# Performance work log

Hardware: AMD Instinct MI355X
Metric: run time of the kernel (lower is better)

## Reference

```python
import jax, jax.numpy as jnp
import numpy as np

N = 2048  # number of graph nodes


def setup_inputs() -> dict:
    key = jax.random.key(0)
    k1, k2, k3, k4 = jax.random.split(key, 4)
    # dense non-negative adjacency / association matrix
    A = jax.random.uniform(k1, (N, N), dtype=jnp.float32)
    # GTConv weights: layer0.conv1, layer0.conv2, layer1.conv1 (each (2,1,1,1))
    w1a = jax.random.normal(k2, (2, 1, 1, 1), dtype=jnp.float32)
    w1b = jax.random.normal(k3, (2, 1, 1, 1), dtype=jnp.float32)
    w2a = jax.random.normal(k4, (2, 1, 1, 1), dtype=jnp.float32)
    return {"A": A, "w1a": w1a, "w1b": w1b, "w2a": w2a}


def _gtconv(A4, w):
    # A4: (1,1,n,n); w: (2,1,1,1). softmax over dim=1 (singleton -> ones),
    # broadcast-multiply -> (2,1,n,n), sum over dim 0 -> (1,n,n)
    sw = jax.nn.softmax(w, axis=1)
    return jnp.sum(A4 * sw, axis=0)


def _norm(H):
    # H: (n,n). H <- diag(deg)^-1 @ (H + I), expressed as a row-scale
    # (identical math to the diagonal mm in the original).
    n = H.shape[0]
    H = H + jnp.eye(n, dtype=H.dtype)
    deg = jnp.sum(H, axis=1)
    deg = jnp.where(deg <= 1e-10, jnp.ones_like(deg), deg)
    return H / deg[:, None]


def reference(A, w1a, w1b, w2a):
    A4 = A[None, None]  # (1,1,n,n) after the forward's unsqueeze + broadcast
    # layer 0 (first=True)
    a = _gtconv(A4, w1a)            # (1,n,n)
    b = _gtconv(A4, w1b)            # (1,n,n)
    H = jnp.matmul(a, b)            # (1,n,n)
    # layer 1 (first=False): normalization of H[0], then bmm with conv(A)
    H_ = _norm(H[0])[None]          # (1,n,n)
    a2 = _gtconv(A4, w2a)           # (1,n,n)
    H2 = jnp.matmul(H_, a2)         # (1,n,n)
    return H2
```

## Files before the change

### kernel.cpp

```cpp
#include <hip/hip_runtime.h>
#include <stdint.h>

#define N 2048
#define TILE 128
#define BK 32

typedef unsigned short u16;
typedef __bf16 bf16x8 __attribute__((ext_vector_type(8)));
typedef unsigned short ushortx8 __attribute__((ext_vector_type(8)));
typedef float floatx4 __attribute__((ext_vector_type(4)));

static __device__ __forceinline__ u16 f2bf(float f) {
  unsigned int u = __builtin_bit_cast(unsigned int, f);
  return (u16)((u + 0x7fffu + ((u >> 16) & 1u)) >> 16);
}
static __device__ __forceinline__ float bf2f(u16 h) {
  unsigned int u = ((unsigned int)h) << 16;
  return __builtin_bit_cast(float, u);
}

static __device__ __forceinline__ void cp16(u16* lds, const u16* g) {
  __builtin_amdgcn_global_load_lds((const __attribute__((address_space(1))) void*)g,
                                   (__attribute__((address_space(3))) void*)lds,
                                   16, 0, 0);
}

__global__ void cast_tr(const float* __restrict__ A, u16* __restrict__ Ab,
                        u16* __restrict__ Abt) {
  __shared__ float tile[32][33];
  const int tx = threadIdx.x, ty = threadIdx.y;
  const int c = blockIdx.x * 32 + tx;
#pragma unroll
  for (int i = 0; i < 4; i++) {
    const int r = blockIdx.y * 32 + ty + i * 8;
    const float v = A[r * N + c];
    Ab[r * N + c] = f2bf(v);
    tile[ty + i * 8][tx] = v;
  }
  __syncthreads();
  const int r2 = blockIdx.y * 32 + tx;
#pragma unroll
  for (int i = 0; i < 4; i++) {
    const int c2 = blockIdx.x * 32 + ty + i * 8;
    Abt[c2 * N + r2] = f2bf(tile[tx][ty + i * 8]);
  }
}

__device__ __forceinline__ void gemm_tile(const u16* __restrict__ L,
                                          const u16* __restrict__ Rt,
                                          floatx4 acc[4][4]) {
  __shared__ __align__(16) u16 As[TILE * BK];
  __shared__ __align__(16) u16 Bs[TILE * BK];

  const int t = threadIdx.x;
  const int row0 = blockIdx.y * TILE;
  const int col0 = blockIdx.x * TILE;

  const int crow = t >> 2;
  const int coff = (t & 3) * 8;
  const u16* gA0 = L + (size_t)(row0 + crow) * N + coff;
  const u16* gA1 = gA0 + (size_t)64 * N;
  const u16* gB0 = Rt + (size_t)(col0 + crow) * N + coff;
  const u16* gB1 = gB0 + (size_t)64 * N;
  u16* lA0 = As + t * 8;
  u16* lA1 = As + 2048 + t * 8;
  u16* lB0 = Bs + t * 8;
  u16* lB1 = Bs + 2048 + t * 8;

  const int lane = t & 63;
  const int w = t >> 6;
  const int wr = (w >> 1) * 64;
  const int wc = (w & 1) * 64;
  const int lr = lane & 15;
  const int q = lane >> 4;

#pragma unroll
  for (int i = 0; i < 4; i++)
#pragma unroll
    for (int j = 0; j < 4; j++) acc[i][j] = (floatx4){0.f, 0.f, 0.f, 0.f};

  for (int k0 = 0; k0 < N; k0 += BK) {
    cp16(lA0, gA0 + k0);
    cp16(lA1, gA1 + k0);
    cp16(lB0, gB0 + k0);
    cp16(lB1, gB1 + k0);
    __syncthreads();

    bf16x8 a[4], b[4];
#pragma unroll
    for (int mt = 0; mt < 4; mt++)
      a[mt] = __builtin_bit_cast(
          bf16x8, *(const ushortx8*)&As[(wr + mt * 16 + lr) * BK + q * 8]);
#pragma unroll
    for (int nt = 0; nt < 4; nt++)
      b[nt] = __builtin_bit_cast(
          bf16x8, *(const ushortx8*)&Bs[(wc + nt * 16 + lr) * BK + q * 8]);
#pragma unroll
    for (int mt = 0; mt < 4; mt++)
#pragma unroll
      for (int nt = 0; nt < 4; nt++)
        acc[mt][nt] = __builtin_amdgcn_mfma_f32_16x16x32_bf16(
            a[mt], b[nt], acc[mt][nt], 0, 0, 0);
    __syncthreads();
  }
}

__global__ __launch_bounds__(256, 2) void gemm_aa(const u16* __restrict__ Ab,
                                                  const u16* __restrict__ Abt,
                                                  u16* __restrict__ Mb) {
  floatx4 acc[4][4];
  gemm_tile(Ab, Abt, acc);
  const int t = threadIdx.x;
  const int lane = t & 63, w = t >> 6;
  const int wr = (w >> 1) * 64, wc = (w & 1) * 64;
  const int lr = lane & 15, q = lane >> 4;
  const int row0 = blockIdx.y * TILE, col0 = blockIdx.x * TILE;
#pragma unroll
  for (int mt = 0; mt < 4; mt++)
#pragma unroll
    for (int r = 0; r < 4; r++) {
      const int rr = row0 + wr + mt * 16 + q * 4 + r;
#pragma unroll
      for (int nt = 0; nt < 4; nt++) {
        const int cc = col0 + wc + nt * 16 + lr;
        Mb[(size_t)rr * N + cc] = f2bf(acc[mt][nt][r]);
      }
    }
}

__global__ void rowsum_k(const u16* __restrict__ Mb, float* __restrict__ rdeg) {
  const int row = blockIdx.x;
  const int t = threadIdx.x;
  const ushortx8 v = *((const ushortx8*)(Mb + (size_t)row * N) + t);
  float s = 0.f;
#pragma unroll
  for (int j = 0; j < 8; j++) s += bf2f(v[j]);
#pragma unroll
  for (int off = 32; off > 0; off >>= 1) s += __shfl_down(s, off, 64);
  __shared__ float ws[4];
  if ((t & 63) == 0) ws[t >> 6] = s;
  __syncthreads();
  if (t == 0) {
    float d = 4.f * (ws[0] + ws[1] + ws[2] + ws[3]) + 1.f;
    if (d <= 1e-10f) d = 1.f;
    rdeg[row] = 1.f / d;
  }
}

__global__ __launch_bounds__(256, 2) void gemm_ma(const u16* __restrict__ Mb,
                                                  const u16* __restrict__ Abt,
                                                  const float* __restrict__ A,
                                                  const float* __restrict__ rdeg,
                                                  float* __restrict__ out) {
  floatx4 acc[4][4];
  gemm_tile(Mb, Abt, acc);
  const int t = threadIdx.x;
  const int lane = t & 63, w = t >> 6;
  const int wr = (w >> 1) * 64, wc = (w & 1) * 64;
  const int lr = lane & 15, q = lane >> 4;
  const int row0 = blockIdx.y * TILE, col0 = blockIdx.x * TILE;
#pragma unroll
  for (int mt = 0; mt < 4; mt++)
#pragma unroll
    for (int r = 0; r < 4; r++) {
      const int rr = row0 + wr + mt * 16 + q * 4 + r;
      const float rd = rdeg[rr];
#pragma unroll
      for (int nt = 0; nt < 4; nt++) {
        const int cc = col0 + wc + nt * 16 + lr;
        out[(size_t)rr * N + cc] =
            (8.f * acc[mt][nt][r] + 2.f * A[(size_t)rr * N + cc]) * rd;
      }
    }
}

extern "C" void kernel_launch(void* const* d_in, const int* in_sizes, int n_in,
                              void* d_out, int out_size, void* d_ws, size_t ws_size,
                              hipStream_t stream) {
  const float* A = (const float*)d_in[0];
  float* out = (float*)d_out;
  char* ws = (char*)d_ws;
  u16* Ab = (u16*)(ws);
  u16* Abt = (u16*)(ws + (size_t)N * N * 2);
  u16* Mb = (u16*)(ws + (size_t)N * N * 4);
  float* rdeg = (float*)(ws + (size_t)N * N * 6);

  cast_tr<<<dim3(N / 32, N / 32), dim3(32, 8), 0, stream>>>(A, Ab, Abt);
  gemm_aa<<<dim3(N / TILE, N / TILE), 256, 0, stream>>>(Ab, Abt, Mb);
  rowsum_k<<<N, 256, 0, stream>>>(Mb, rdeg);
  gemm_ma<<<dim3(N / TILE, N / TILE), 256, 0, stream>>>(Mb, Abt, A, rdeg, out);
}
```

Baseline: 160.3 us.

## Split-K both GEMMs and fuse row-degree computation into partial-sum reduction

Result: slower. 184.7 us (+15.2%).

```diff
diff --git a/kernel.cpp b/kernel.cpp
--- a/kernel.cpp
+++ b/kernel.cpp
@@ -4,10 +4,12 @@
 #define N 2048
 #define TILE 128
 #define BK 32
+#define NN ((size_t)N * (size_t)N)
 
 typedef unsigned short u16;
 typedef __bf16 bf16x8 __attribute__((ext_vector_type(8)));
 typedef unsigned short ushortx8 __attribute__((ext_vector_type(8)));
+typedef unsigned short ushortx4 __attribute__((ext_vector_type(4)));
 typedef float floatx4 __attribute__((ext_vector_type(4)));
 
 static __device__ __forceinline__ u16 f2bf(float f) {
@@ -46,15 +48,18 @@
   }
 }
 
-__device__ __forceinline__ void gemm_tile(const u16* __restrict__ L,
-                                          const u16* __restrict__ Rt,
-                                          floatx4 acc[4][4]) {
+__global__ __launch_bounds__(256, 2) void gemm_sk(const u16* __restrict__ L,
+                                                  const u16* __restrict__ Rt,
+                                                  u16* __restrict__ P,
+                                                  int ksl) {
   __shared__ __align__(16) u16 As[TILE * BK];
   __shared__ __align__(16) u16 Bs[TILE * BK];
 
   const int t = threadIdx.x;
   const int row0 = blockIdx.y * TILE;
   const int col0 = blockIdx.x * TILE;
+  const int kbeg = blockIdx.z * ksl;
+  const int kend = kbeg + ksl;
 
   const int crow = t >> 2;
   const int coff = (t & 3) * 8;
@@ -74,12 +79,13 @@
   const int lr = lane & 15;
   const int q = lane >> 4;
 
+  floatx4 acc[4][4];
 #pragma unroll
   for (int i = 0; i < 4; i++)
 #pragma unroll
     for (int j = 0; j < 4; j++) acc[i][j] = (floatx4){0.f, 0.f, 0.f, 0.f};
 
-  for (int k0 = 0; k0 < N; k0 += BK) {
+  for (int k0 = kbeg; k0 < kend; k0 += BK) {
     cp16(lA0, gA0 + k0);
     cp16(lA1, gA1 + k0);
     cp16(lB0, gB0 + k0);
@@ -103,75 +109,109 @@
             a[mt], b[nt], acc[mt][nt], 0, 0, 0);
     __syncthreads();
   }
-}
-
-__global__ __launch_bounds__(256, 2) void gemm_aa(const u16* __restrict__ Ab,
-                                                  const u16* __restrict__ Abt,
-                                                  u16* __restrict__ Mb) {
-  floatx4 acc[4][4];
-  gemm_tile(Ab, Abt, acc);
+
+  u16* Pp = P + (size_t)blockIdx.z * NN +
+            (size_t)(blockIdx.y * gridDim.x + blockIdx.x) * (TILE * TILE) +
+            (size_t)w * 4096 + (size_t)lane * 4;
+#pragma unroll
+  for (int mt = 0; mt < 4; mt++)
+#pragma unroll
+    for (int nt = 0; nt < 4; nt++) {
+      ushortx4 v;
+#pragma unroll
+      for (int r = 0; r < 4; r++) v[r] = f2bf(acc[mt][nt][r]);
+      *(ushortx4*)(Pp + (mt * 4 + nt) * 256) = v;
+    }
+}
+
+__global__ __launch_bounds__(256) void reduce1(const u16* __restrict__ P,
+                                               u16* __restrict__ Mb,
+                                               float* __restrict__ deg,
+                                               int nz) {
+  __shared__ float rs[TILE];
   const int t = threadIdx.x;
+  const int blk = blockIdx.x;
+  const int bx = blk & 15, by = blk >> 4;
+  const int row0 = by * TILE, col0 = bx * TILE;
   const int lane = t & 63, w = t >> 6;
   const int wr = (w >> 1) * 64, wc = (w & 1) * 64;
   const int lr = lane & 15, q = lane >> 4;
-  const int row0 = blockIdx.y * TILE, col0 = blockIdx.x * TILE;
+  if (t < TILE) rs[t] = 0.f;
+  __syncthreads();
+
+  const u16* Pp = P + (size_t)blk * (TILE * TILE) + (size_t)w * 4096 +
+                  (size_t)lane * 4;
+  float trs[4][4];
+#pragma unroll
+  for (int i = 0; i < 4; i++)
+#pragma unroll
+    for (int j = 0; j < 4; j++) trs[i][j] = 0.f;
+
+#pragma unroll
+  for (int p = 0; p < 16; p++) {
+    const int mt = p >> 2, nt = p & 3;
+    float s[4] = {0.f, 0.f, 0.f, 0.f};
+    for (int z = 0; z < nz; z++) {
+      ushortx4 v = *(const ushortx4*)(Pp + (size_t)z * NN + p * 256);
+#pragma unroll
+      for (int r = 0; r < 4; r++) s[r] += bf2f(v[r]);
+    }
+    const int rr = row0 + wr + mt * 16 + q * 4;
+    const int cc = col0 + wc + nt * 16 + lr;
+#pragma unroll
+    for (int r = 0; r < 4; r++) {
+      Mb[(size_t)(rr + r) * N + cc] = f2bf(s[r]);
+      trs[mt][r] += s[r];
+    }
+  }
 #pragma unroll
   for (int mt = 0; mt < 4; mt++)
 #pragma unroll
-    for (int r = 0; r < 4; r++) {
-      const int rr = row0 + wr + mt * 16 + q * 4 + r;
-#pragma unroll
-      for (int nt = 0; nt < 4; nt++) {
-        const int cc = col0 + wc + nt * 16 + lr;
-        Mb[(size_t)rr * N + cc] = f2bf(acc[mt][nt][r]);
-      }
-    }
-}
-
-__global__ void rowsum_k(const u16* __restrict__ Mb, float* __restrict__ rdeg) {
-  const int row = blockIdx.x;
+    for (int r = 0; r < 4; r++)
+      atomicAdd(&rs[wr + mt * 16 + q * 4 + r], trs[mt][r]);
+  __syncthreads();
+  if (t < TILE) atomicAdd(&deg[row0 + t], rs[t]);
+}
+
+__global__ __launch_bounds__(256) void reduce2(const u16* __restrict__ Q,
+                                               const float* __restrict__ A,
+                                               const float* __restrict__ deg,
+                                               float* __restrict__ out,
+                                               int nz) {
+  __shared__ float rdeg[TILE];
   const int t = threadIdx.x;
-  const ushortx8 v = *((const ushortx8*)(Mb + (size_t)row * N) + t);
-  float s = 0.f;
-#pragma unroll
-  for (int j = 0; j < 8; j++) s += bf2f(v[j]);
-#pragma unroll
-  for (int off = 32; off > 0; off >>= 1) s += __shfl_down(s, off, 64);
-  __shared__ float ws[4];
-  if ((t & 63) == 0) ws[t >> 6] = s;
-  __syncthreads();
-  if (t == 0) {
-    float d = 4.f * (ws[0] + ws[1] + ws[2] + ws[3]) + 1.f;
-    if (d <= 1e-10f) d = 1.f;
-    rdeg[row] = 1.f / d;
-  }
-}
-
-__global__ __launch_bounds__(256, 2) void gemm_ma(const u16* __restrict__ Mb,
-                                                  const u16* __restrict__ Abt,
-                                                  const float* __restrict__ A,
-                                                  const float* __restrict__ rdeg,
-                                                  float* __restrict__ out) {
-  floatx4 acc[4][4];
-  gemm_tile(Mb, Abt, acc);
-  const int t = threadIdx.x;
+  const int blk = blockIdx.x;
+  const int bx = blk & 15, by = blk >> 4;
+  const int row0 = by * TILE, col0 = bx * TILE;
   const int lane = t & 63, w = t >> 6;
   const int wr = (w >> 1) * 64, wc = (w & 1) * 64;
   const int lr = lane & 15, q = lane >> 4;
-  const int row0 = blockIdx.y * TILE, col0 = blockIdx.x * TILE;
-#pragma unroll
-  for (int mt = 0; mt < 4; mt++)
-#pragma unroll
-    for (int r = 0; r < 4; r++) {
-      const int rr = row0 + wr + mt * 16 + q * 4 + r;
-      const float rd = rdeg[rr];
-#pragma unroll
-      for (int nt = 0; nt < 4; nt++) {
-        const int cc = col0 + wc + nt * 16 + lr;
-        out[(size_t)rr * N + cc] =
-            (8.f * acc[mt][nt][r] + 2.f * A[(size_t)rr * N + cc]) * rd;
-      }
-    }
+  if (t < TILE) {
+    float d = 4.f * deg[row0 + t] + 1.f;
+    if (d <= 1e-10f) d = 1.f;
+    rdeg[t] = 1.f / d;
+  }
+  __syncthreads();
+
+  const u16* Qp = Q + (size_t)blk * (TILE * TILE) + (size_t)w * 4096 +
+                  (size_t)lane * 4;
+#pragma unroll
+  for (int p = 0; p < 16; p++) {
+    const int mt = p >> 2, nt = p & 3;
+    float s[4] = {0.f, 0.f, 0.f, 0.f};
+    for (int z = 0; z < nz; z++) {
+      ushortx4 v = *(const ushortx4*)(Qp + (size_t)z * NN + p * 256);
+#pragma unroll
+      for (int r = 0; r < 4; r++) s[r] += bf2f(v[r]);
+    }
+    const int rr = row0 + wr + mt * 16 + q * 4;
+    const int cc = col0 + wc + nt * 16 + lr;
+#pragma unroll
+    for (int r = 0; r < 4; r++)
+      out[(size_t)(rr + r) * N + cc] =
+          (8.f * s[r] + 2.f * A[(size_t)(rr + r) * N + cc]) *
+          rdeg[wr + mt * 16 + q * 4 + r];
+  }
 }
 
 extern "C" void kernel_launch(void* const* d_in, const int* in_sizes, int n_in,
@@ -180,13 +220,19 @@
   const float* A = (const float*)d_in[0];
   float* out = (float*)d_out;
   char* ws = (char*)d_ws;
-  u16* Ab = (u16*)(ws);
-  u16* Abt = (u16*)(ws + (size_t)N * N * 2);
-  u16* Mb = (u16*)(ws + (size_t)N * N * 4);
-  float* rdeg = (float*)(ws + (size_t)N * N * 6);
-
+  u16* Ab = (u16*)ws;
+  u16* Abt = (u16*)(ws + NN * 2);
+  u16* Mb = (u16*)(ws + NN * 4);
+  u16* P = (u16*)(ws + NN * 6);
+
+  const size_t need4 = NN * 6 + NN * 2 * 4 + (size_t)N * 4;
+  const int nz = (ws_size >= need4) ? 4 : 1;
+  float* deg = (float*)(ws + NN * 6 + NN * 2 * (size_t)nz);
+
+  hipMemsetAsync(deg, 0, N * sizeof(float), stream);
   cast_tr<<<dim3(N / 32, N / 32), dim3(32, 8), 0, stream>>>(A, Ab, Abt);
-  gemm_aa<<<dim3(N / TILE, N / TILE), 256, 0, stream>>>(Ab, Abt, Mb);
-  rowsum_k<<<N, 256, 0, stream>>>(Mb, rdeg);
-  gemm_ma<<<dim3(N / TILE, N / TILE), 256, 0, stream>>>(Mb, Abt, A, rdeg, out);
-}
+  gemm_sk<<<dim3(16, 16, nz), 256, 0, stream>>>(Ab, Abt, P, N / nz);
+  reduce1<<<256, 256, 0, stream>>>(P, Mb, deg, nz);
+  gemm_sk<<<dim3(16, 16, nz), 256, 0, stream>>>(Mb, Abt, P, N / nz);
+  reduce2<<<256, 256, 0, stream>>>(P, A, deg, out, nz);
+}
```

## Pipeline GEMM K-loop with 4-stage LDS ring and async global_load_lds prefetch

Applied to the files above, without the earlier changes.

Result: slower. 164.2 us (+2.4%).

```diff
diff --git a/kernel.cpp b/kernel.cpp
--- a/kernel.cpp
+++ b/kernel.cpp
@@ -4,6 +4,9 @@
 #define N 2048
 #define TILE 128
 #define BK 32
+#define KI (N / BK)
+#define STAGES 4
+#define NN ((size_t)N * (size_t)N)
 
 typedef unsigned short u16;
 typedef __bf16 bf16x8 __attribute__((ext_vector_type(8)));
@@ -49,8 +52,8 @@
 __device__ __forceinline__ void gemm_tile(const u16* __restrict__ L,
                                           const u16* __restrict__ Rt,
                                           floatx4 acc[4][4]) {
-  __shared__ __align__(16) u16 As[TILE * BK];
-  __shared__ __align__(16) u16 Bs[TILE * BK];
+  __shared__ __align__(16) u16 As[STAGES][TILE * BK];
+  __shared__ __align__(16) u16 Bs[STAGES][TILE * BK];
 
   const int t = threadIdx.x;
   const int row0 = blockIdx.y * TILE;
@@ -62,10 +65,6 @@
   const u16* gA1 = gA0 + (size_t)64 * N;
   const u16* gB0 = Rt + (size_t)(col0 + crow) * N + coff;
   const u16* gB1 = gB0 + (size_t)64 * N;
-  u16* lA0 = As + t * 8;
-  u16* lA1 = As + 2048 + t * 8;
-  u16* lB0 = Bs + t * 8;
-  u16* lB1 = Bs + 2048 + t * 8;
 
   const int lane = t & 63;
   const int w = t >> 6;
@@ -79,29 +78,49 @@
 #pragma unroll
     for (int j = 0; j < 4; j++) acc[i][j] = (floatx4){0.f, 0.f, 0.f, 0.f};
 
-  for (int k0 = 0; k0 < N; k0 += BK) {
-    cp16(lA0, gA0 + k0);
-    cp16(lA1, gA1 + k0);
-    cp16(lB0, gB0 + k0);
-    cp16(lB1, gB1 + k0);
-    __syncthreads();
-
+#pragma unroll
+  for (int s = 0; s < 3; s++) {
+    const int k0 = s * BK;
+    cp16(&As[s][t * 8], gA0 + k0);
+    cp16(&As[s][2048 + t * 8], gA1 + k0);
+    cp16(&Bs[s][t * 8], gB0 + k0);
+    cp16(&Bs[s][2048 + t * 8], gB1 + k0);
+  }
+
+  for (int i = 0; i < KI; ++i) {
+    if (i < KI - 2)
+      asm volatile("s_waitcnt vmcnt(8)" ::: "memory");
+    else if (i == KI - 2)
+      asm volatile("s_waitcnt vmcnt(4)" ::: "memory");
+    else
+      asm volatile("s_waitcnt vmcnt(0)" ::: "memory");
+    asm volatile("s_barrier" ::: "memory");
+
+    if (i + 3 < KI) {
+      const int s = (i + 3) & (STAGES - 1);
+      const int k0 = (i + 3) * BK;
+      cp16(&As[s][t * 8], gA0 + k0);
+      cp16(&As[s][2048 + t * 8], gA1 + k0);
+      cp16(&Bs[s][t * 8], gB0 + k0);
+      cp16(&Bs[s][2048 + t * 8], gB1 + k0);
+    }
+
+    const int cur = i & (STAGES - 1);
     bf16x8 a[4], b[4];
 #pragma unroll
     for (int mt = 0; mt < 4; mt++)
       a[mt] = __builtin_bit_cast(
-          bf16x8, *(const ushortx8*)&As[(wr + mt * 16 + lr) * BK + q * 8]);
+          bf16x8, *(const ushortx8*)&As[cur][(wr + mt * 16 + lr) * BK + q * 8]);
 #pragma unroll
     for (int nt = 0; nt < 4; nt++)
       b[nt] = __builtin_bit_cast(
-          bf16x8, *(const ushortx8*)&Bs[(wc + nt * 16 + lr) * BK + q * 8]);
+          bf16x8, *(const ushortx8*)&Bs[cur][(wc + nt * 16 + lr) * BK + q * 8]);
 #pragma unroll
     for (int mt = 0; mt < 4; mt++)
 #pragma unroll
       for (int nt = 0; nt < 4; nt++)
         acc[mt][nt] = __builtin_amdgcn_mfma_f32_16x16x32_bf16(
             a[mt], b[nt], acc[mt][nt], 0, 0, 0);
-    __syncthreads();
   }
 }
 
@@ -180,10 +199,10 @@
   const float* A = (const float*)d_in[0];
   float* out = (float*)d_out;
   char* ws = (char*)d_ws;
-  u16* Ab = (u16*)(ws);
-  u16* Abt = (u16*)(ws + (size_t)N * N * 2);
-  u16* Mb = (u16*)(ws + (size_t)N * N * 4);
-  float* rdeg = (float*)(ws + (size_t)N * N * 6);
+  u16* Ab = (u16*)ws;
+  u16* Abt = (u16*)(ws + NN * 2);
+  u16* Mb = (u16*)(ws + NN * 4);
+  float* rdeg = (float*)(ws + NN * 6);
 
   cast_tr<<<dim3(N / 32, N / 32), dim3(32, 8), 0, stream>>>(A, Ab, Abt);
   gemm_aa<<<dim3(N / TILE, N / TILE), 256, 0, stream>>>(Ab, Abt, Mb);
```

## Pipeline GEMM loads through registers with double-buffered padded LDS and 8 waves

Applied to the files above, without the earlier changes.

Measured after the change: 138.7 us. 13.5% less time.

```diff
diff --git a/kernel.cpp b/kernel.cpp
--- a/kernel.cpp
+++ b/kernel.cpp
@@ -4,6 +4,9 @@
 #define N 2048
 #define TILE 128
 #define BK 32
+#define KI (N / BK)
+#define LDSW 40
+#define NN ((size_t)N * (size_t)N)
 
 typedef unsigned short u16;
 typedef __bf16 bf16x8 __attribute__((ext_vector_type(8)));
@@ -17,12 +20,6 @@
 static __device__ __forceinline__ float bf2f(u16 h) {
   unsigned int u = ((unsigned int)h) << 16;
   return __builtin_bit_cast(float, u);
-}
-
-static __device__ __forceinline__ void cp16(u16* lds, const u16* g) {
-  __builtin_amdgcn_global_load_lds((const __attribute__((address_space(1))) void*)g,
-                                   (__attribute__((address_space(3))) void*)lds,
-                                   16, 0, 0);
 }
 
 __global__ void cast_tr(const float* __restrict__ A, u16* __restrict__ Ab,
@@ -46,73 +43,88 @@
   }
 }
 
-__device__ __forceinline__ void gemm_tile(const u16* __restrict__ L,
+__device__ __forceinline__ void gemm_core(const u16* __restrict__ L,
                                           const u16* __restrict__ Rt,
-                                          floatx4 acc[4][4]) {
-  __shared__ __align__(16) u16 As[TILE * BK];
-  __shared__ __align__(16) u16 Bs[TILE * BK];
+                                          floatx4 acc[4][2]) {
+  __shared__ __align__(16) u16 As[2][TILE * LDSW];
+  __shared__ __align__(16) u16 Bs[2][TILE * LDSW];
 
   const int t = threadIdx.x;
   const int row0 = blockIdx.y * TILE;
   const int col0 = blockIdx.x * TILE;
 
-  const int crow = t >> 2;
-  const int coff = (t & 3) * 8;
-  const u16* gA0 = L + (size_t)(row0 + crow) * N + coff;
-  const u16* gA1 = gA0 + (size_t)64 * N;
-  const u16* gB0 = Rt + (size_t)(col0 + crow) * N + coff;
-  const u16* gB1 = gB0 + (size_t)64 * N;
-  u16* lA0 = As + t * 8;
-  u16* lA1 = As + 2048 + t * 8;
-  u16* lB0 = Bs + t * 8;
-  u16* lB1 = Bs + 2048 + t * 8;
+  const int srow = t >> 2;
+  const int sc = (t & 3) * 8;
+  const u16* gA = L + (size_t)(row0 + srow) * N + sc;
+  const u16* gB = Rt + (size_t)(col0 + srow) * N + sc;
+  const int woff = srow * LDSW + sc;
 
   const int lane = t & 63;
   const int w = t >> 6;
-  const int wr = (w >> 1) * 64;
-  const int wc = (w & 1) * 64;
+  const int wr = (w >> 2) * 64;
+  const int wc = (w & 3) * 32;
   const int lr = lane & 15;
   const int q = lane >> 4;
+  const int aoff = (wr + lr) * LDSW + q * 8;
+  const int boff = (wc + lr) * LDSW + q * 8;
 
 #pragma unroll
   for (int i = 0; i < 4; i++)
 #pragma unroll
-    for (int j = 0; j < 4; j++) acc[i][j] = (floatx4){0.f, 0.f, 0.f, 0.f};
-
-  for (int k0 = 0; k0 < N; k0 += BK) {
-    cp16(lA0, gA0 + k0);
-    cp16(lA1, gA1 + k0);
-    cp16(lB0, gB0 + k0);
-    cp16(lB1, gB1 + k0);
-    __syncthreads();
-
-    bf16x8 a[4], b[4];
-#pragma unroll
-    for (int mt = 0; mt < 4; mt++)
-      a[mt] = __builtin_bit_cast(
-          bf16x8, *(const ushortx8*)&As[(wr + mt * 16 + lr) * BK + q * 8]);
-#pragma unroll
-    for (int nt = 0; nt < 4; nt++)
-      b[nt] = __builtin_bit_cast(
-          bf16x8, *(const ushortx8*)&Bs[(wc + nt * 16 + lr) * BK + q * 8]);
-#pragma unroll
-    for (int mt = 0; mt < 4; mt++)
-#pragma unroll
-      for (int nt = 0; nt < 4; nt++)
-        acc[mt][nt] = __builtin_amdgcn_mfma_f32_16x16x32_bf16(
-            a[mt], b[nt], acc[mt][nt], 0, 0, 0);
-    __syncthreads();
-  }
-}
-
-__global__ __launch_bounds__(256, 2) void gemm_aa(const u16* __restrict__ Ab,
+    for (int j = 0; j < 2; j++) acc[i][j] = (floatx4){0.f, 0.f, 0.f, 0.f};
+
+  ushortx8 rA[4], rB[4];
+#pragma unroll
+  for (int s = 0; s < 3; s++) {
+    rA[s] = *(const ushortx8*)(gA + s * BK);
+    rB[s] = *(const ushortx8*)(gB + s * BK);
+  }
+  *(ushortx8*)(&As[0][woff]) = rA[0];
+  *(ushortx8*)(&Bs[0][woff]) = rB[0];
+  __syncthreads();
+
+#define GSTEP(i, s, cur, nxt)                                                \
+  {                                                                          \
+    if ((i) + 3 < KI) {                                                      \
+      rA[((s) + 3) & 3] = *(const ushortx8*)(gA + ((i) + 3) * BK);           \
+      rB[((s) + 3) & 3] = *(const ushortx8*)(gB + ((i) + 3) * BK);           \
+    }                                                                        \
+    bf16x8 af[4], bfr[2];                                                    \
+    _Pragma("unroll") for (int mt = 0; mt < 4; mt++) af[mt] =                \
+        __builtin_bit_cast(bf16x8,                                           \
+                           *(const ushortx8*)&As[cur][aoff + mt * 16 * LDSW]); \
+    _Pragma("unroll") for (int nt = 0; nt < 2; nt++) bfr[nt] =               \
+        __builtin_bit_cast(bf16x8,                                           \
+                           *(const ushortx8*)&Bs[cur][boff + nt * 16 * LDSW]); \
+    _Pragma("unroll") for (int mt = 0; mt < 4; mt++)                         \
+        _Pragma("unroll") for (int nt = 0; nt < 2; nt++) acc[mt][nt] =       \
+            __builtin_amdgcn_mfma_f32_16x16x32_bf16(af[mt], bfr[nt],         \
+                                                    acc[mt][nt], 0, 0, 0);   \
+    __syncthreads();   \
+    if ((i) + 1 < KI) {                                                      \
+      *(ushortx8*)(&As[nxt][woff]) = rA[((s) + 1) & 3];                      \
+      *(ushortx8*)(&Bs[nxt][woff]) = rB[((s) + 1) & 3];                      \
+    }                                                                        \
+    __syncthreads();                      \
+  }
+
+  for (int io = 0; io < KI; io += 4) {
+    GSTEP(io + 0, 0, 0, 1)
+    GSTEP(io + 1, 1, 1, 0)
+    GSTEP(io + 2, 2, 0, 1)
+    GSTEP(io + 3, 3, 1, 0)
+  }
+#undef GSTEP
+}
+
+__global__ __launch_bounds__(512, 2) void gemm_aa(const u16* __restrict__ Ab,
                                                   const u16* __restrict__ Abt,
                                                   u16* __restrict__ Mb) {
-  floatx4 acc[4][4];
-  gemm_tile(Ab, Abt, acc);
+  floatx4 acc[4][2];
+  gemm_core(Ab, Abt, acc);
   const int t = threadIdx.x;
   const int lane = t & 63, w = t >> 6;
-  const int wr = (w >> 1) * 64, wc = (w & 1) * 64;
+  const int wr = (w >> 2) * 64, wc = (w & 3) * 32;
   const int lr = lane & 15, q = lane >> 4;
   const int row0 = blockIdx.y * TILE, col0 = blockIdx.x * TILE;
 #pragma unroll
@@ -121,7 +133,7 @@
     for (int r = 0; r < 4; r++) {
       const int rr = row0 + wr + mt * 16 + q * 4 + r;
 #pragma unroll
-      for (int nt = 0; nt < 4; nt++) {
+      for (int nt = 0; nt < 2; nt++) {
         const int cc = col0 + wc + nt * 16 + lr;
         Mb[(size_t)rr * N + cc] = f2bf(acc[mt][nt][r]);
       }
@@ -147,16 +159,16 @@
   }
 }
 
-__global__ __launch_bounds__(256, 2) void gemm_ma(const u16* __restrict__ Mb,
+__global__ __launch_bounds__(512, 2) void gemm_ma(const u16* __restrict__ Mb,
                                                   const u16* __restrict__ Abt,
                                                   const float* __restrict__ A,
                                                   const float* __restrict__ rdeg,
                                                   float* __restrict__ out) {
-  floatx4 acc[4][4];
-  gemm_tile(Mb, Abt, acc);
+  floatx4 acc[4][2];
+  gemm_core(Mb, Abt, acc);
   const int t = threadIdx.x;
   const int lane = t & 63, w = t >> 6;
-  const int wr = (w >> 1) * 64, wc = (w & 1) * 64;
+  const int wr = (w >> 2) * 64, wc = (w & 3) * 32;
   const int lr = lane & 15, q = lane >> 4;
   const int row0 = blockIdx.y * TILE, col0 = blockIdx.x * TILE;
 #pragma unroll
@@ -166,7 +178,7 @@
       const int rr = row0 + wr + mt * 16 + q * 4 + r;
       const float rd = rdeg[rr];
 #pragma unroll
-      for (int nt = 0; nt < 4; nt++) {
+      for (int nt = 0; nt < 2; nt++) {
         const int cc = col0 + wc + nt * 16 + lr;
         out[(size_t)rr * N + cc] =
             (8.f * acc[mt][nt][r] + 2.f * A[(size_t)rr * N + cc]) * rd;
@@ -180,13 +192,13 @@
   const float* A = (const float*)d_in[0];
   float* out = (float*)d_out;
   char* ws = (char*)d_ws;
-  u16* Ab = (u16*)(ws);
-  u16* Abt = (u16*)(ws + (size_t)N * N * 2);
-  u16* Mb = (u16*)(ws + (size_t)N * N * 4);
-  float* rdeg = (float*)(ws + (size_t)N * N * 6);
+  u16* Ab = (u16*)ws;
+  u16* Abt = (u16*)(ws + NN * 2);
+  u16* Mb = (u16*)(ws + NN * 4);
+  float* rdeg = (float*)(ws + NN * 6);
 
   cast_tr<<<dim3(N / 32, N / 32), dim3(32, 8), 0, stream>>>(A, Ab, Abt);
-  gemm_aa<<<dim3(N / TILE, N / TILE), 256, 0, stream>>>(Ab, Abt, Mb);
+  gemm_aa<<<dim3(N / TILE, N / TILE), 512, 0, stream>>>(Ab, Abt, Mb);
   rowsum_k<<<N, 256, 0, stream>>>(Mb, rdeg);
-  gemm_ma<<<dim3(N / TILE, N / TILE), 256, 0, stream>>>(Mb, Abt, A, rdeg, out);
-}
+  gemm_ma<<<dim3(N / TILE, N / TILE), 512, 0, stream>>>(Mb, Abt, A, rdeg, out);
+}
```
